# Kernel tuning notes

Measured on AMD Instinct MI355X. Metric: run time of the kernel, lower is better.

The kernel has to match this reference:

```python
import jax, jax.numpy as jnp
import numpy as np

D_MODEL = 3072
NUM_EXPERTS = 8
TOP_K = 2
BATCH, SEQ = 4, 4096


def setup_inputs() -> dict:
    key = jax.random.key(0)
    kx, kw, kb = jax.random.split(key, 3)
    x = jax.random.normal(kx, (BATCH, SEQ, D_MODEL), dtype=jnp.float32)
    W = jax.random.normal(kw, (NUM_EXPERTS, D_MODEL), dtype=jnp.float32) * (1.0 / np.sqrt(D_MODEL))
    b = jax.random.normal(kb, (NUM_EXPERTS,), dtype=jnp.float32) * 0.02
    return {"x": x, "W": W, "b": b}


def reference(x, W, b):
    # Linear gate: [B, S, D] x [E, D]^T -> [B, S, E]
    logits = jnp.einsum("bsd,ed->bse", x, W) + b
    gate_scores = jax.nn.softmax(logits, axis=-1)
    # top-k over experts
    topk_values, topk_indices = jax.lax.top_k(gate_scores, TOP_K)
    # renormalize the selected scores with a second softmax
    topk_values = jax.nn.softmax(topk_values, axis=-1)
    return (topk_values, topk_indices)
```

## Files before the change

### kernel.cpp

```cpp
#include <hip/hip_runtime.h>
#include <stdint.h>


#define NTOK   16384
#define DMODEL 3072
#define NEXP   8
#define TPB    256
#define TOKW   4
#define TOKB   16
#define STF    128
#define NST    (DMODEL / STF)

#define GATE_COMPUTE(WR, XR)                                          \
  {                                                                   \
    _Pragma("unroll")                                                 \
    for (int p = 0; p < TOKW; ++p) {                                  \
      const float4 xv = XR[p];                                        \
      _Pragma("unroll")                                               \
      for (int e = 0; e < 4; ++e)                                     \
        acc[p][e] = fmaf(xv.x, WR[e].x,                               \
                    fmaf(xv.y, WR[e].y,                               \
                    fmaf(xv.z, WR[e].z,                               \
                    fmaf(xv.w, WR[e].w, acc[p][e]))));                \
    }                                                                 \
  }

__global__ __launch_bounds__(TPB, 4) void gate_fused4(
    const float* __restrict__ x, const float* __restrict__ W,
    const float* __restrict__ bias, float* __restrict__ out) {
  const int tid  = threadIdx.x;
  const int wv   = tid >> 6;
  const int lane = tid & 63;
  const int tg   = lane & 1;
  const int sl   = lane >> 1;
  const int tokBase = blockIdx.x * TOKB + wv * TOKW;

  const float* px[TOKW];
#pragma unroll
  for (int p = 0; p < TOKW; ++p)
    px[p] = x + (size_t)(tokBase + p) * DMODEL + sl * 4;

  const float* pw[4];
#pragma unroll
  for (int e = 0; e < 4; ++e)
    pw[e] = W + (size_t)(tg * 4 + e) * DMODEL + sl * 4;

  float acc[TOKW][4];
#pragma unroll
  for (int p = 0; p < TOKW; ++p)
#pragma unroll
    for (int e = 0; e < 4; ++e) acc[p][e] = 0.f;

  float4 wa[4], wb[4], xa[TOKW], xb[TOKW];
#pragma unroll
  for (int e = 0; e < 4; ++e) wa[e] = *(const float4*)(pw[e]);
#pragma unroll
  for (int p = 0; p < TOKW; ++p) xa[p] = *(const float4*)(px[p]);

#pragma unroll 1
  for (int s = 0; s < NST; s += 2) {
#pragma unroll
    for (int e = 0; e < 4; ++e)
      wb[e] = *(const float4*)(pw[e] + (s + 1) * STF);
#pragma unroll
    for (int p = 0; p < TOKW; ++p)
      xb[p] = *(const float4*)(px[p] + (s + 1) * STF);

    GATE_COMPUTE(wa, xa);

    if (s + 2 < NST) {
#pragma unroll
      for (int e = 0; e < 4; ++e)
        wa[e] = *(const float4*)(pw[e] + (s + 2) * STF);
#pragma unroll
      for (int p = 0; p < TOKW; ++p)
        xa[p] = *(const float4*)(px[p] + (s + 2) * STF);
    }

    GATE_COMPUTE(wb, xb);
  }

#pragma unroll
  for (int p = 0; p < TOKW; ++p)
#pragma unroll
    for (int e = 0; e < 4; ++e) {
      float v = acc[p][e];
      v += __shfl_xor(v, 2, 64);
      v += __shfl_xor(v, 4, 64);
      v += __shfl_xor(v, 8, 64);
      v += __shfl_xor(v, 16, 64);
      v += __shfl_xor(v, 32, 64);
      acc[p][e] = v;
    }

  float own[4], send[4];
#pragma unroll
  for (int p = 0; p < TOKW; ++p) {
    const bool isown  = (lane & 3) == p;
    const bool issend = ((lane ^ 1) & 3) == p;
#pragma unroll
    for (int e = 0; e < 4; ++e) {
      if (isown)  own[e]  = acc[p][e];
      if (issend) send[e] = acc[p][e];
    }
  }
  float other[4];
#pragma unroll
  for (int e = 0; e < 4; ++e) other[e] = __shfl_xor(send[e], 1, 64);

  if (lane < TOKW) {
    const float4 b0 = *(const float4*)bias;
    const float4 b1 = *(const float4*)(bias + 4);

    float l[NEXP];
    if ((lane & 1) == 0) {
      l[0] = own[0] + b0.x;   l[1] = own[1] + b0.y;
      l[2] = own[2] + b0.z;   l[3] = own[3] + b0.w;
      l[4] = other[0] + b1.x; l[5] = other[1] + b1.y;
      l[6] = other[2] + b1.z; l[7] = other[3] + b1.w;
    } else {
      l[0] = other[0] + b0.x; l[1] = other[1] + b0.y;
      l[2] = other[2] + b0.z; l[3] = other[3] + b0.w;
      l[4] = own[0] + b1.x;   l[5] = own[1] + b1.y;
      l[6] = own[2] + b1.z;   l[7] = own[3] + b1.w;
    }

    float m = l[0];
#pragma unroll
    for (int e = 1; e < NEXP; ++e) m = fmaxf(m, l[e]);

    float p8[NEXP];
    float ssum = 0.f;
#pragma unroll
    for (int e = 0; e < NEXP; ++e) {
      p8[e] = expf(l[e] - m);
      ssum += p8[e];
    }
    const float inv = 1.f / ssum;
#pragma unroll
    for (int e = 0; e < NEXP; ++e) p8[e] *= inv;

    int i1 = 0;
    float v1 = p8[0];
#pragma unroll
    for (int e = 1; e < NEXP; ++e) {
      if (p8[e] > v1) { v1 = p8[e]; i1 = e; }
    }
    int i2 = -1;
    float v2 = -1.f;
#pragma unroll
    for (int e = 0; e < NEXP; ++e) {
      if (e == i1) continue;
      if (p8[e] > v2) { v2 = p8[e]; i2 = e; }
    }

    const float e2 = expf(v2 - v1);
    const float r = 1.f / (1.f + e2);

    const int tok = tokBase + lane;
    *(float2*)(out + (size_t)tok * 2) = make_float2(r, e2 * r);
    *(float2*)(out + 2 * NTOK + (size_t)tok * 2) =
        make_float2((float)i1, (float)i2);
  }
}

extern "C" void kernel_launch(void* const* d_in, const int* in_sizes, int n_in,
                              void* d_out, int out_size, void* d_ws,
                              size_t ws_size, hipStream_t stream) {
  const float* x = (const float*)d_in[0];
  const float* W = (const float*)d_in[1];
  const float* b = (const float*)d_in[2];
  float* out = (float*)d_out;
  (void)d_ws; (void)ws_size;

  gate_fused4<<<dim3(NTOK / TOKB), TPB, 0, stream>>>(x, W, b, out);
}
```

Before: 281.4 us.

## Stage gate weights in LDS in two halves and double block size

Each block now preloads the 8x3072 gate weight matrix into registers and stages it through shared memory in two halves of 48 KB, instead of every wave streaming W from global memory for each stripe. Block size doubles to 512 threads, so each block covers 32 tokens and the staging cost is spread over more tokens. Per-wave global traffic then becomes only x loads. The cost is two extra barriers, a large LDS footprint that may limit blocks per CU, and higher register pressure from the preloaded weight halves.

```diff
diff --git a/kernel.cpp b/kernel.cpp
--- a/kernel.cpp
+++ b/kernel.cpp
@@ -5,11 +5,15 @@
 #define NTOK   16384
 #define DMODEL 3072
 #define NEXP   8
-#define TPB    256
+#define TPB    512
+#define NWAVE  (TPB / 64)
 #define TOKW   4
-#define TOKB   16
+#define TOKB   (NWAVE * TOKW)
 #define STF    128
 #define NST    (DMODEL / STF)
+#define HALF   (NST / 2)
+#define W4H    (NEXP * HALF * 32)
+#define W4PT   (W4H / TPB)
 
 #define GATE_COMPUTE(WR, XR)                                          \
   {                                                                   \
@@ -25,9 +29,32 @@
     }                                                                 \
   }
 
-__global__ __launch_bounds__(TPB, 4) void gate_fused4(
+#define GATE_ITER(SL, S)                                              \
+  {                                                                   \
+    _Pragma("unroll")                                                 \
+    for (int p = 0; p < TOKW; ++p)                                    \
+      xb[p] = *(const float4*)(px[p] + ((S) + 1) * STF);              \
+    float4 w4[4];                                                     \
+    _Pragma("unroll")                                                 \
+    for (int e = 0; e < 4; ++e)                                       \
+      w4[e] = sw4[(SL) * 256 + (tg * 4 + e) * 32 + sl];               \
+    GATE_COMPUTE(w4, xa);                                             \
+    if ((S) + 2 < NST) {                                              \
+      _Pragma("unroll")                                               \
+      for (int p = 0; p < TOKW; ++p)                                  \
+        xa[p] = *(const float4*)(px[p] + ((S) + 2) * STF);            \
+    }                                                                 \
+    _Pragma("unroll")                                                 \
+    for (int e = 0; e < 4; ++e)                                       \
+      w4[e] = sw4[((SL) + 1) * 256 + (tg * 4 + e) * 32 + sl];         \
+    GATE_COMPUTE(w4, xb);                                             \
+  }
+
+__global__ __launch_bounds__(TPB, 4) void gate_fused6(
     const float* __restrict__ x, const float* __restrict__ W,
     const float* __restrict__ bias, float* __restrict__ out) {
+  __shared__ float4 sw4[W4H];
+
   const int tid  = threadIdx.x;
   const int wv   = tid >> 6;
   const int lane = tid & 63;
@@ -35,15 +62,38 @@
   const int sl   = lane >> 1;
   const int tokBase = blockIdx.x * TOKB + wv * TOKW;
 
+  const float4* Wf4 = (const float4*)W;
+
+  float4 wrA[W4PT], wrB[W4PT];
+#pragma unroll
+  for (int k = 0; k < W4PT; ++k) {
+    const int L = tid + k * TPB;
+    const int e = L / 384, r = L - e * 384;
+    wrA[k] = Wf4[e * 768 + r];
+  }
+#pragma unroll
+  for (int k = 0; k < W4PT; ++k) {
+    const int L = tid + k * TPB;
+    const int e = L / 384, r = L - e * 384;
+    wrB[k] = Wf4[e * 768 + 384 + r];
+  }
+
   const float* px[TOKW];
 #pragma unroll
   for (int p = 0; p < TOKW; ++p)
     px[p] = x + (size_t)(tokBase + p) * DMODEL + sl * 4;
 
-  const float* pw[4];
-#pragma unroll
-  for (int e = 0; e < 4; ++e)
-    pw[e] = W + (size_t)(tg * 4 + e) * DMODEL + sl * 4;
+  float4 xa[TOKW], xb[TOKW];
+#pragma unroll
+  for (int p = 0; p < TOKW; ++p) xa[p] = *(const float4*)(px[p]);
+
+#pragma unroll
+  for (int k = 0; k < W4PT; ++k) {
+    const int L = tid + k * TPB;
+    const int e = L / 384, r = L - e * 384;
+    sw4[(r >> 5) * 256 + e * 32 + (r & 31)] = wrA[k];
+  }
+  __syncthreads();
 
   float acc[TOKW][4];
 #pragma unroll
@@ -51,33 +101,23 @@
 #pragma unroll
     for (int e = 0; e < 4; ++e) acc[p][e] = 0.f;
 
-  float4 wa[4], wb[4], xa[TOKW], xb[TOKW];
-#pragma unroll
-  for (int e = 0; e < 4; ++e) wa[e] = *(const float4*)(pw[e]);
-#pragma unroll
-  for (int p = 0; p < TOKW; ++p) xa[p] = *(const float4*)(px[p]);
-
 #pragma unroll 1
-  for (int s = 0; s < NST; s += 2) {
-#pragma unroll
-    for (int e = 0; e < 4; ++e)
-      wb[e] = *(const float4*)(pw[e] + (s + 1) * STF);
-#pragma unroll
-    for (int p = 0; p < TOKW; ++p)
-      xb[p] = *(const float4*)(px[p] + (s + 1) * STF);
-
-    GATE_COMPUTE(wa, xa);
-
-    if (s + 2 < NST) {
-#pragma unroll
-      for (int e = 0; e < 4; ++e)
-        wa[e] = *(const float4*)(pw[e] + (s + 2) * STF);
-#pragma unroll
-      for (int p = 0; p < TOKW; ++p)
-        xa[p] = *(const float4*)(px[p] + (s + 2) * STF);
-    }
-
-    GATE_COMPUTE(wb, xb);
+  for (int s = 0; s < HALF; s += 2) {
+    GATE_ITER(s, s);
+  }
+
+  __syncthreads();
+#pragma unroll
+  for (int k = 0; k < W4PT; ++k) {
+    const int L = tid + k * TPB;
+    const int e = L / 384, r = L - e * 384;
+    sw4[(r >> 5) * 256 + e * 32 + (r & 31)] = wrB[k];
+  }
+  __syncthreads();
+
+#pragma unroll 1
+  for (int s = 0; s < HALF; s += 2) {
+    GATE_ITER(s, HALF + s);
   }
 
 #pragma unroll
@@ -173,5 +213,5 @@
   float* out = (float*)d_out;
   (void)d_ws; (void)ws_size;
 
-  gate_fused4<<<dim3(NTOK / TOKB), TPB, 0, stream>>>(x, W, b, out);
+  gate_fused6<<<dim3(NTOK / TOKB), TPB, 0, stream>>>(x, W, b, out);
 }
```

New measurement: 289.5 us. 1.03x slower.
